# Kernel tuning notes

Measured on AMD Instinct MI355X. Metric: run time of the kernel, lower is better.

## Reference

```python
import jax, jax.numpy as jnp
import numpy as np

C, D, H, W = 4, 16, 1024, 1024
REF = 3
MAX_SHIFT = (0.1, 0.1)


def setup_inputs() -> dict:
    key = jax.random.key(0)
    kx, ks = jax.random.split(key)
    x = jax.random.normal(kx, (C, D, H, W), dtype=jnp.float32)
    # Replicate torch: max_shift = rand(2)*ms*2 - ms; /= (D-1); shift[i] = (i-ref)*max_shift*[H,W] -> long
    ms = jnp.asarray(MAX_SHIFT, jnp.float32)
    u = jax.random.uniform(ks, (2,), jnp.float32) * ms * 2.0 - ms
    u = u / (D - 1)
    s = (jnp.arange(D, dtype=jnp.float32) - REF)[:, None] * u[None, :]  # [D,2] fractional
    shift = (s * jnp.asarray([H, W], jnp.float32)).astype(jnp.int32)     # truncation matches .long()
    return {"x": x, "shift": shift}


def reference(x, shift):
    # Fused equivalent of the per-slice torch.roll loop (fill='none'):
    # out[c, d, i, j] = x[c, d, (i - shift[d,0]) % H, (j - shift[d,1]) % W]
    # shift[REF] == 0 by construction, so the ref slice is untouched.
    _, D_, H_, W_ = x.shape
    row = (jnp.arange(H_)[None, :] - shift[:, 0:1]) % H_  # [D, H]
    col = (jnp.arange(W_)[None, :] - shift[:, 1:2]) % W_  # [D, W]
    d = jnp.arange(D_)
    return x[:, d[:, None, None], row[:, :, None], col[:, None, :]]  # [C, D, H, W]
```

## Files before the change

kernel.cpp:

```cpp
#include <hip/hip_runtime.h>


#define CC 4
#define DD 16
#define HH 1024
#define WW 1024

typedef float floatx4 __attribute__((ext_vector_type(4)));

struct __align__(4) f4u { float x, y, z, w; };

__global__ __launch_bounds__(256)
void PixelShift_kernel(const float* __restrict__ x,
                       const int* __restrict__ shift,
                       float* __restrict__ out) {
    __shared__ int s_sh[2 * DD];
    if (threadIdx.x < 2 * DD) s_sh[threadIdx.x] = shift[threadIdx.x];
    __syncthreads();

    const int total4 = CC * DD * HH * (WW / 4);
    const int stride = gridDim.x * blockDim.x;
#pragma unroll 4
    for (int t = blockIdx.x * blockDim.x + threadIdx.x; t < total4; t += stride) {
        const int j4 = t & (WW / 4 - 1);
        const int r  = t >> 8;
        const int i  = r & (HH - 1);
        const int cd = r >> 10;
        const int d  = cd & (DD - 1);

        const int s0 = s_sh[2 * d];
        const int s1 = s_sh[2 * d + 1];

        const int si = (i - s0) & (HH - 1);
        const float* __restrict__ row = x + ((size_t)cd * HH + si) * WW;

        const int js = ((j4 << 2) - s1) & (WW - 1);

        floatx4 v;
        if (js <= WW - 4) {
            f4u u = *reinterpret_cast<const f4u*>(row + js);
            v.x = u.x; v.y = u.y; v.z = u.z; v.w = u.w;
        } else {
            v.x = row[js];
            v.y = row[(js + 1) & (WW - 1)];
            v.z = row[(js + 2) & (WW - 1)];
            v.w = row[(js + 3) & (WW - 1)];
        }

        __builtin_nontemporal_store(v, reinterpret_cast<floatx4*>(out) + t);
    }
}

extern "C" void kernel_launch(void* const* d_in, const int* in_sizes, int n_in,
                              void* d_out, int out_size, void* d_ws, size_t ws_size,
                              hipStream_t stream) {
    const float* x     = (const float*)d_in[0];
    const int*   shift = (const int*)d_in[1];
    float*       out   = (float*)d_out;

    const int blocks  = 2048;
    const int threads = 256;
    PixelShift_kernel<<<blocks, threads, 0, stream>>>(x, shift, out);
}
```

Before: 86.76 us.

## Use aligned vector loads with wavefront shuffles for misaligned column shifts

Unaligned 16-byte loads are replaced by aligned floatx4 loads; the misaligned output is rebuilt from the next lane's data via __shfl_down, and the last lane issues one extra load. The loop is batched so four independent loads are in flight before the stores. This aims to remove unaligned or split memory accesses and raise memory-level parallelism, at the cost of cross-lane shuffles and extra registers. The shuffle is correct only when srem is the same across a wavefront, which holds because shift is per depth slice and the 64 lanes share a row.

```diff
diff --git a/kernel.cpp b/kernel.cpp
--- a/kernel.cpp
+++ b/kernel.cpp
@@ -8,8 +8,6 @@
 
 typedef float floatx4 __attribute__((ext_vector_type(4)));
 
-struct __align__(4) f4u { float x, y, z, w; };
-
 __global__ __launch_bounds__(256)
 void PixelShift_kernel(const float* __restrict__ x,
                        const int* __restrict__ shift,
@@ -18,36 +16,61 @@
     if (threadIdx.x < 2 * DD) s_sh[threadIdx.x] = shift[threadIdx.x];
     __syncthreads();
 
-    const int total4 = CC * DD * HH * (WW / 4);
+    const int lane   = threadIdx.x & 63;
+    const int tid    = blockIdx.x * blockDim.x + threadIdx.x;
     const int stride = gridDim.x * blockDim.x;
-#pragma unroll 4
-    for (int t = blockIdx.x * blockDim.x + threadIdx.x; t < total4; t += stride) {
-        const int j4 = t & (WW / 4 - 1);
-        const int r  = t >> 8;
-        const int i  = r & (HH - 1);
-        const int cd = r >> 10;
-        const int d  = cd & (DD - 1);
+    constexpr int TOTAL4 = CC * DD * HH * (WW / 4);
+    constexpr int BATCH  = 4;
 
-        const int s0 = s_sh[2 * d];
-        const int s1 = s_sh[2 * d + 1];
+    for (int t0 = tid; t0 < TOTAL4; t0 += stride * BATCH) {
+        floatx4 A[BATCH], P[BATCH];
+        int srem[BATCH], tA[BATCH];
 
-        const int si = (i - s0) & (HH - 1);
-        const float* __restrict__ row = x + ((size_t)cd * HH + si) * WW;
+#pragma unroll
+        for (int k = 0; k < BATCH; ++k) {
+            const int t  = t0 + k * stride;
+            tA[k] = t;
+            const int j4 = t & (WW / 4 - 1);
+            const int r  = t >> 8;
+            const int i  = r & (HH - 1);
+            const int cd = r >> 10;
+            const int d  = cd & (DD - 1);
 
-        const int js = ((j4 << 2) - s1) & (WW - 1);
+            const int s0 = s_sh[2 * d];
+            const int s1 = s_sh[2 * d + 1];
 
-        floatx4 v;
-        if (js <= WW - 4) {
-            f4u u = *reinterpret_cast<const f4u*>(row + js);
-            v.x = u.x; v.y = u.y; v.z = u.z; v.w = u.w;
-        } else {
-            v.x = row[js];
-            v.y = row[(js + 1) & (WW - 1)];
-            v.z = row[(js + 2) & (WW - 1)];
-            v.w = row[(js + 3) & (WW - 1)];
+            const int si = (i - s0) & (HH - 1);
+            const floatx4* __restrict__ row4 =
+                reinterpret_cast<const floatx4*>(x + ((size_t)cd * HH + si) * WW);
+
+            const int js = ((j4 << 2) - s1) & (WW - 1);
+            const int a0 = js >> 2;
+            srem[k] = js & 3;
+
+            A[k] = row4[a0];
+            if (lane == 63 && srem[k] != 0)
+                P[k] = row4[(a0 + 1) & (WW / 4 - 1)];
         }
 
-        __builtin_nontemporal_store(v, reinterpret_cast<floatx4*>(out) + t);
+#pragma unroll
+        for (int k = 0; k < BATCH; ++k) {
+            const floatx4 Ak = A[k];
+            floatx4 v;
+            if (srem[k] == 0) {
+                v = Ak;
+            } else {
+                floatx4 B;
+                B.x = __shfl_down(Ak.x, 1);
+                B.y = __shfl_down(Ak.y, 1);
+                B.z = __shfl_down(Ak.z, 1);
+                B.w = __shfl_down(Ak.w, 1);
+                if (lane == 63) B = P[k];
+                if (srem[k] == 1)      v = (floatx4){Ak.y, Ak.z, Ak.w, B.x};
+                else if (srem[k] == 2) v = (floatx4){Ak.z, Ak.w, B.x, B.y};
+                else                   v = (floatx4){Ak.w, B.x, B.y, B.z};
+            }
+            __builtin_nontemporal_store(v, reinterpret_cast<floatx4*>(out) + tA[k]);
+        }
     }
 }
 
```

Result: no change. 85.12 us (-1.9%).
